# Kernel optimization log

Measured on AMD Instinct MI355X. Metric: run time of the kernel, lower is better.

The kernel has to match this reference:

```python
import jax, jax.numpy as jnp
import numpy as np

TAU = 0.5
EPS = 1e-8


def _mlp(x, W1, b1, W2, b2):
    # torch nn.Linear: y = x @ W.T + b
    h = jax.nn.elu(x @ W1.T + b1)
    return h @ W2.T + b2


def setup_inputs() -> dict:
    key = jax.random.key(0)
    ks = jax.random.split(key, 10)
    N, D = 8192, 256
    gain = 1.414
    std = gain * np.sqrt(2.0 / (D + D))  # xavier_normal_
    inp = {
        "z1": jax.random.normal(ks[0], (N, D), dtype=jnp.float32),
        "z2": jax.random.normal(ks[1], (N, D), dtype=jnp.float32),
        "W1c": std * jax.random.normal(ks[2], (D, D), dtype=jnp.float32),
        "b1c": jnp.zeros((D,), dtype=jnp.float32),
        "W2c": std * jax.random.normal(ks[3], (D, D), dtype=jnp.float32),
        "b2c": jnp.zeros((D,), dtype=jnp.float32),
        "W1k": std * jax.random.normal(ks[4], (D, D), dtype=jnp.float32),
        "b1k": jnp.zeros((D,), dtype=jnp.float32),
        "W2k": std * jax.random.normal(ks[5], (D, D), dtype=jnp.float32),
        "b2k": jnp.zeros((D,), dtype=jnp.float32),
        "cl_size": N,
    }
    return inp


def reference(z1, z2, W1c, b1c, W2c, b2c, W1k, b1k, W2k, b2k, cl_size):
    z1p = _mlp(z1, W1c, b1c, W2c, b2c)  # [N, D]
    z2p = _mlp(z2, W1k, b1k, W2k, b2k)  # [N, D]
    n1 = jnp.linalg.norm(z1p, axis=-1, keepdims=True)  # [N, 1]
    n2 = jnp.linalg.norm(z2p, axis=-1, keepdims=True)  # [N, 1]
    dot = z1p @ z2p.T                                  # [N, N]
    sim = jnp.exp(dot / (n1 * n2.T) / TAU)
    sim = sim / (jnp.sum(sim, axis=1, keepdims=True) + EPS)
    pos = jnp.diagonal(sim)                            # diag(sim * I).sum(-1)
    return -jnp.mean(jnp.log(pos))
```

## Files before the change

kernel.cpp:

```cpp
#include <hip/hip_runtime.h>

typedef __bf16 bf16;
typedef __bf16 bf16x8 __attribute__((ext_vector_type(8)));
typedef __bf16 bf16x4v __attribute__((ext_vector_type(4)));
typedef float  f32x4  __attribute__((ext_vector_type(4)));

#define NROWS 8192
#define DDIM  256
#define TAU_INV 2.0f
#define KAPPA 2.8853900817779268f
#define LN2 0.6931471805599453f
#define EPS 1e-8f

#define AS1C(p) ((const __attribute__((address_space(1))) void*)(p))
#define AS3(p)  ((__attribute__((address_space(3))) void*)(p))

static __device__ __forceinline__ bf16x8 cvt8(f32x4 a, f32x4 b) {
  bf16x8 o;
  o[0] = (bf16)a[0]; o[1] = (bf16)a[1]; o[2] = (bf16)a[2]; o[3] = (bf16)a[3];
  o[4] = (bf16)b[0]; o[5] = (bf16)b[1]; o[6] = (bf16)b[2]; o[7] = (bf16)b[3];
  return o;
}

__global__ __launch_bounds__(256) void cast4_kernel(
    const float* __restrict__ s0, const float* __restrict__ s1,
    const float* __restrict__ s2, const float* __restrict__ s3,
    bf16* __restrict__ dst) {
  const float* s = blockIdx.y == 0 ? s0 : blockIdx.y == 1 ? s1 : blockIdx.y == 2 ? s2 : s3;
  bf16* d = dst + (size_t)blockIdx.y * 65536;
  int i = blockIdx.x * 256 + threadIdx.x;
  f32x4 v = ((const f32x4*)s)[i];
  bf16x4v o;
  o[0] = (bf16)v[0]; o[1] = (bf16)v[1]; o[2] = (bf16)v[2]; o[3] = (bf16)v[3];
  ((bf16x4v*)d)[i] = o;
}

__global__ __launch_bounds__(512, 1) void mlp_norm_kernel(
    const float* __restrict__ z1f, const float* __restrict__ z2f,
    const bf16* __restrict__ wq,
    const float* __restrict__ b1c, const float* __restrict__ b2c,
    const float* __restrict__ b1k, const float* __restrict__ b2k,
    bf16* __restrict__ outA, bf16* __restrict__ outB)
{
  const int view = blockIdx.y;
  const float* xf = view ? z2f : z1f;
  const bf16*  w1 = wq + (size_t)view * 131072;
  const bf16*  w2 = w1 + 65536;
  const float* b1 = view ? b1k : b1c;
  const float* b2 = view ? b2k : b2c;
  bf16* out = view ? outB : outA;
  const float osc = view ? 1.0f : KAPPA;

  __shared__ __align__(16) char xs[64 * 512];
  __shared__ __align__(16) char hs[64 * 512];
  __shared__ float sspart[8][64];

  const int tid  = threadIdx.x;
  const int lane = tid & 63;
  const int w    = tid >> 6;
  const int c    = lane & 15;
  const int g    = lane >> 4;
  const int r0   = blockIdx.x * 64;
  const int colw = w * 32;

#pragma unroll
  for (int k = 0; k < 4; ++k) {
    int gid = k * 512 + tid;
    int row = gid >> 5, cg = gid & 31;
    const f32x4* p = (const f32x4*)(xf + (size_t)(r0 + row) * DDIM + cg * 8);
    *(bf16x8*)(xs + row * 512 + ((cg * 16) ^ ((row & 7) << 4))) = cvt8(p[0], p[1]);
  }
  __syncthreads();

  float b1v[2], b2v[2];
#pragma unroll
  for (int ct = 0; ct < 2; ++ct) {
    b1v[ct] = b1[colw + ct * 16 + c];
    b2v[ct] = b2[colw + ct * 16 + c];
  }

  const int aswz = (c & 7) << 4;
  const bf16* w1base = w1 + (size_t)(colw + c) * DDIM + g * 8;
  const bf16* w2base = w2 + (size_t)(colw + c) * DDIM + g * 8;

  f32x4 acc[2][4];
  const f32x4 fz = {0.f, 0.f, 0.f, 0.f};
#pragma unroll
  for (int ct = 0; ct < 2; ++ct)
#pragma unroll
    for (int mt = 0; mt < 4; ++mt) acc[ct][mt] = fz;

  bf16x8 wcur[2], wnxt[2];
#pragma unroll
  for (int ct = 0; ct < 2; ++ct)
    wcur[ct] = *(const bf16x8*)(w1base + (size_t)ct * 16 * DDIM);
#pragma unroll
  for (int ks = 0; ks < 8; ++ks) {
    if (ks < 7) {
#pragma unroll
      for (int ct = 0; ct < 2; ++ct)
        wnxt[ct] = *(const bf16x8*)(w1base + (size_t)ct * 16 * DDIM + (ks + 1) * 32);
    }
    bf16x8 af[4];
#pragma unroll
    for (int mt = 0; mt < 4; ++mt)
      af[mt] = *(const bf16x8*)(xs + (mt * 16 + c) * 512 + ((ks * 64 + g * 16) ^ aswz));
#pragma unroll
    for (int ct = 0; ct < 2; ++ct)
#pragma unroll
      for (int mt = 0; mt < 4; ++mt)
        acc[ct][mt] = __builtin_amdgcn_mfma_f32_16x16x32_bf16(af[mt], wcur[ct], acc[ct][mt], 0, 0, 0);
#pragma unroll
    for (int ct = 0; ct < 2; ++ct) wcur[ct] = wnxt[ct];
  }

#pragma unroll
  for (int ct = 0; ct < 2; ++ct)
#pragma unroll
    for (int mt = 0; mt < 4; ++mt)
#pragma unroll
      for (int r = 0; r < 4; ++r) {
        float pre = acc[ct][mt][r] + b1v[ct];
        float h = pre > 0.0f ? pre : (__expf(pre) - 1.0f);
        int row = mt * 16 + g * 4 + r;
        int cb = (colw + ct * 16 + c) * 2;
        *(bf16*)(hs + row * 512 + (cb ^ ((row & 7) << 4))) = (bf16)h;
      }
  __syncthreads();

#pragma unroll
  for (int ct = 0; ct < 2; ++ct)
#pragma unroll
    for (int mt = 0; mt < 4; ++mt) acc[ct][mt] = fz;

#pragma unroll
  for (int ct = 0; ct < 2; ++ct)
    wcur[ct] = *(const bf16x8*)(w2base + (size_t)ct * 16 * DDIM);
#pragma unroll
  for (int ks = 0; ks < 8; ++ks) {
    if (ks < 7) {
#pragma unroll
      for (int ct = 0; ct < 2; ++ct)
        wnxt[ct] = *(const bf16x8*)(w2base + (size_t)ct * 16 * DDIM + (ks + 1) * 32);
    }
    bf16x8 af[4];
#pragma unroll
    for (int mt = 0; mt < 4; ++mt)
      af[mt] = *(const bf16x8*)(hs + (mt * 16 + c) * 512 + ((ks * 64 + g * 16) ^ aswz));
#pragma unroll
    for (int ct = 0; ct < 2; ++ct)
#pragma unroll
      for (int mt = 0; mt < 4; ++mt)
        acc[ct][mt] = __builtin_amdgcn_mfma_f32_16x16x32_bf16(af[mt], wcur[ct], acc[ct][mt], 0, 0, 0);
#pragma unroll
    for (int ct = 0; ct < 2; ++ct) wcur[ct] = wnxt[ct];
  }

  float ss[4][4];
#pragma unroll
  for (int mt = 0; mt < 4; ++mt)
#pragma unroll
    for (int r = 0; r < 4; ++r) ss[mt][r] = 0.f;
#pragma unroll
  for (int ct = 0; ct < 2; ++ct)
#pragma unroll
    for (int mt = 0; mt < 4; ++mt)
#pragma unroll
      for (int r = 0; r < 4; ++r) {
        float z = acc[ct][mt][r] + b2v[ct];
        acc[ct][mt][r] = z;
        ss[mt][r] += z * z;
      }
#pragma unroll
  for (int m = 1; m < 16; m <<= 1)
#pragma unroll
    for (int mt = 0; mt < 4; ++mt)
#pragma unroll
      for (int r = 0; r < 4; ++r) ss[mt][r] += __shfl_xor(ss[mt][r], m, 64);

  if (c == 0) {
#pragma unroll
    for (int mt = 0; mt < 4; ++mt)
#pragma unroll
      for (int r = 0; r < 4; ++r) sspart[w][mt * 16 + g * 4 + r] = ss[mt][r];
  }
  __syncthreads();

#pragma unroll
  for (int mt = 0; mt < 4; ++mt)
#pragma unroll
    for (int r = 0; r < 4; ++r) {
      int row = mt * 16 + g * 4 + r;
      float s = (sspart[0][row] + sspart[1][row]) + (sspart[2][row] + sspart[3][row])
              + (sspart[4][row] + sspart[5][row]) + (sspart[6][row] + sspart[7][row]);
      float rinv = osc / sqrtf(s);
#pragma unroll
      for (int ct = 0; ct < 2; ++ct)
        out[(size_t)(r0 + row) * DDIM + colw + ct * 16 + c] = (bf16)(acc[ct][mt][r] * rinv);
    }
}

__global__ __launch_bounds__(256, 2) void lse_kernel(
    const bf16* __restrict__ A, const bf16* __restrict__ B,
    float* __restrict__ partial, float* __restrict__ diagdot)
{
  __shared__ __align__(16) char As[128 * 128];
  __shared__ __align__(16) char Bs[128 * 128];

  const int tid  = threadIdx.x;
  const int lane = tid & 63;
  const int w    = tid >> 6;
  const int c    = lane & 15;
  const int g    = lane >> 4;
  const int brow = blockIdx.y * 128;
  const int bcol = blockIdx.x * 128;
  const int wrow = (w >> 1) * 64;
  const int wcol = (w & 1) * 64;

  f32x4 acc[4][4];
  const f32x4 fz = {0.f, 0.f, 0.f, 0.f};
#pragma unroll
  for (int i = 0; i < 4; ++i)
#pragma unroll
    for (int j = 0; j < 4; ++j) acc[i][j] = fz;

  for (int kt = 0; kt < 4; ++kt) {
#pragma unroll
    for (int it = 0; it < 4; ++it) {
      int slot = it * 256 + tid;
      int row = slot >> 3, q = slot & 7;
      int col = kt * 64 + ((q ^ (row & 7)) * 8);
      __builtin_amdgcn_global_load_lds(AS1C(A + (size_t)(brow + row) * DDIM + col),
                                       AS3(As + (it * 256 + w * 64) * 16), 16, 0, 0);
      __builtin_amdgcn_global_load_lds(AS1C(B + (size_t)(bcol + row) * DDIM + col),
                                       AS3(Bs + (it * 256 + w * 64) * 16), 16, 0, 0);
    }
    __syncthreads();
#pragma unroll
    for (int sk = 0; sk < 2; ++sk) {
      bf16x8 af[4], bfv[4];
#pragma unroll
      for (int mt = 0; mt < 4; ++mt) {
        int rl = wrow + mt * 16 + c;
        af[mt] = *(const bf16x8*)(As + rl * 128 + ((sk * 64 + g * 16) ^ ((rl & 7) << 4)));
      }
#pragma unroll
      for (int ct = 0; ct < 4; ++ct) {
        int rl = wcol + ct * 16 + c;
        bfv[ct] = *(const bf16x8*)(Bs + rl * 128 + ((sk * 64 + g * 16) ^ ((rl & 7) << 4)));
      }
#pragma unroll
      for (int mt = 0; mt < 4; ++mt)
#pragma unroll
        for (int ct = 0; ct < 4; ++ct)
          acc[mt][ct] = __builtin_amdgcn_mfma_f32_16x16x32_bf16(af[mt], bfv[ct], acc[mt][ct], 0, 0, 0);
    }
    __syncthreads();
  }

  if (blockIdx.x == blockIdx.y && (w == 0 || w == 3) && (c >> 2) == g) {
#pragma unroll
    for (int mt = 0; mt < 4; ++mt) {
      f32x4 a = acc[mt][mt];
      int r = c & 3;
      float dv = (r == 0) ? a[0] : (r == 1) ? a[1] : (r == 2) ? a[2] : a[3];
      diagdot[brow + wrow + mt * 16 + c] = dv;
    }
  }

  float rs[4][4];
#pragma unroll
  for (int mt = 0; mt < 4; ++mt)
#pragma unroll
    for (int r = 0; r < 4; ++r) rs[mt][r] = 0.f;
#pragma unroll
  for (int mt = 0; mt < 4; ++mt)
#pragma unroll
    for (int ct = 0; ct < 4; ++ct)
#pragma unroll
      for (int r = 0; r < 4; ++r) rs[mt][r] += __builtin_amdgcn_exp2f(acc[mt][ct][r]);
#pragma unroll
  for (int m = 1; m < 16; m <<= 1)
#pragma unroll
    for (int mt = 0; mt < 4; ++mt)
#pragma unroll
      for (int r = 0; r < 4; ++r) rs[mt][r] += __shfl_xor(rs[mt][r], m, 64);

  if (c == 0) {
    int cb2 = blockIdx.x * 2 + (w & 1);
#pragma unroll
    for (int mt = 0; mt < 4; ++mt)
#pragma unroll
      for (int r = 0; r < 4; ++r) {
        int grow = brow + wrow + mt * 16 + g * 4 + r;
        partial[(size_t)grow * 128 + cb2] = rs[mt][r];
      }
  }
}

__global__ __launch_bounds__(256) void rowfinal_kernel(
    const float* __restrict__ partial, const float* __restrict__ diagdot,
    float* __restrict__ blocksum)
{
  int gid = blockIdx.x * 256 + threadIdx.x;
  int row = gid >> 2, q = gid & 3;
  const f32x4* p = (const f32x4*)(partial + (size_t)row * 128 + q * 32);
  float s = 0.f;
#pragma unroll
  for (int i = 0; i < 8; ++i) {
    f32x4 v = p[i];
    s += (v[0] + v[1]) + (v[2] + v[3]);
  }
  s += __shfl_xor(s, 1, 64);
  s += __shfl_xor(s, 2, 64);
  float term = (q == 0) ? (logf(s + EPS) - diagdot[row] * LN2) : 0.f;
#pragma unroll
  for (int m = 1; m < 64; m <<= 1) term += __shfl_xor(term, m, 64);
  __shared__ float part[4];
  if ((threadIdx.x & 63) == 0) part[threadIdx.x >> 6] = term;
  __syncthreads();
  if (threadIdx.x == 0) blocksum[blockIdx.x] = part[0] + part[1] + part[2] + part[3];
}

__global__ __launch_bounds__(128) void final_kernel(const float* __restrict__ blocksum,
                                                    float* __restrict__ out)
{
  int tid = threadIdx.x;
  float s = blocksum[tid];
#pragma unroll
  for (int m = 1; m < 64; m <<= 1) s += __shfl_xor(s, m, 64);
  __shared__ float p[2];
  if ((tid & 63) == 0) p[tid >> 6] = s;
  __syncthreads();
  if (tid == 0) out[0] = (p[0] + p[1]) * (1.0f / NROWS);
}

extern "C" void kernel_launch(void* const* d_in, const int* in_sizes, int n_in,
                              void* d_out, int out_size, void* d_ws, size_t ws_size,
                              hipStream_t stream) {
  const float* z1  = (const float*)d_in[0];
  const float* z2  = (const float*)d_in[1];
  const float* W1c = (const float*)d_in[2];
  const float* b1c = (const float*)d_in[3];
  const float* W2c = (const float*)d_in[4];
  const float* b2c = (const float*)d_in[5];
  const float* W1k = (const float*)d_in[6];
  const float* b1k = (const float*)d_in[7];
  const float* W2k = (const float*)d_in[8];
  const float* b2k = (const float*)d_in[9];

  char* ws = (char*)d_ws;
  bf16*  aU       = (bf16*)(ws);
  bf16*  bU       = (bf16*)(ws + (size_t)4  * 1024 * 1024);
  float* partial  = (float*)(ws + (size_t)8  * 1024 * 1024);
  float* diagdot  = (float*)(ws + (size_t)12 * 1024 * 1024);
  float* blocksum = (float*)(ws + (size_t)12 * 1024 * 1024 + 64 * 1024);
  bf16*  wq       = (bf16*)(ws + (size_t)13 * 1024 * 1024);

  cast4_kernel<<<dim3(64, 4), 256, 0, stream>>>(W1c, W2c, W1k, W2k, wq);

  mlp_norm_kernel<<<dim3(NROWS / 64, 2), 512, 0, stream>>>(
      z1, z2, wq, b1c, b2c, b1k, b2k, aU, bU);

  lse_kernel<<<dim3(NROWS / 128, NROWS / 128), 256, 0, stream>>>(aU, bU, partial, diagdot);

  rowfinal_kernel<<<128, 256, 0, stream>>>(partial, diagdot, blocksum);
  final_kernel<<<1, 128, 0, stream>>>(blocksum, (float*)d_out);
}
```

Baseline: 75.94 us.

## Quantize normalized embeddings to FP8 and use FP8 MFMA for similarity GEMM

```diff
diff --git a/kernel.cpp b/kernel.cpp
--- a/kernel.cpp
+++ b/kernel.cpp
@@ -1,4 +1,5 @@
 #include <hip/hip_runtime.h>
+#include <hip/hip_fp8.h>
 
 typedef __bf16 bf16;
 typedef __bf16 bf16x8 __attribute__((ext_vector_type(8)));
@@ -20,6 +21,11 @@
   o[0] = (bf16)a[0]; o[1] = (bf16)a[1]; o[2] = (bf16)a[2]; o[3] = (bf16)a[3];
   o[4] = (bf16)b[0]; o[5] = (bf16)b[1]; o[6] = (bf16)b[2]; o[7] = (bf16)b[3];
   return o;
+}
+
+static __device__ __forceinline__ unsigned char f2fp8(float x) {
+  __hip_fp8_e4m3 q(x);
+  return (unsigned char)q.__x;
 }
 
 __global__ __launch_bounds__(256) void cast4_kernel(
@@ -40,7 +46,7 @@
     const bf16* __restrict__ wq,
     const float* __restrict__ b1c, const float* __restrict__ b2c,
     const float* __restrict__ b1k, const float* __restrict__ b2k,
-    bf16* __restrict__ outA, bf16* __restrict__ outB)
+    unsigned char* __restrict__ outA, unsigned char* __restrict__ outB)
 {
   const int view = blockIdx.y;
   const float* xf = view ? z2f : z1f;
@@ -48,7 +54,7 @@
   const bf16*  w2 = w1 + 65536;
   const float* b1 = view ? b1k : b1c;
   const float* b2 = view ? b2k : b2c;
-  bf16* out = view ? outB : outA;
+  unsigned char* out = view ? outB : outA;
   const float osc = view ? 1.0f : KAPPA;
 
   __shared__ __align__(16) char xs[64 * 512];
@@ -196,16 +202,16 @@
       float rinv = osc / sqrtf(s);
 #pragma unroll
       for (int ct = 0; ct < 2; ++ct)
-        out[(size_t)(r0 + row) * DDIM + colw + ct * 16 + c] = (bf16)(acc[ct][mt][r] * rinv);
+        out[(size_t)(r0 + row) * DDIM + colw + ct * 16 + c] = f2fp8(acc[ct][mt][r] * rinv);
     }
 }
 
 __global__ __launch_bounds__(256, 2) void lse_kernel(
-    const bf16* __restrict__ A, const bf16* __restrict__ B,
+    const unsigned char* __restrict__ A, const unsigned char* __restrict__ B,
     float* __restrict__ partial, float* __restrict__ diagdot)
 {
-  __shared__ __align__(16) char As[128 * 128];
-  __shared__ __align__(16) char Bs[128 * 128];
+  __shared__ __align__(16) char As[128 * 64];
+  __shared__ __align__(16) char Bs[128 * 64];
 
   const int tid  = threadIdx.x;
   const int lane = tid & 63;
@@ -226,34 +232,36 @@
 
   for (int kt = 0; kt < 4; ++kt) {
 #pragma unroll
-    for (int it = 0; it < 4; ++it) {
+    for (int it = 0; it < 2; ++it) {
       int slot = it * 256 + tid;
-      int row = slot >> 3, q = slot & 7;
-      int col = kt * 64 + ((q ^ (row & 7)) * 8);
+      int row = slot >> 2, q = slot & 3;
+      int col = kt * 64 + ((q ^ (row & 3)) << 4);
       __builtin_amdgcn_global_load_lds(AS1C(A + (size_t)(brow + row) * DDIM + col),
-                                       AS3(As + (it * 256 + w * 64) * 16), 16, 0, 0);
+                                       AS3(As + slot * 16), 16, 0, 0);
       __builtin_amdgcn_global_load_lds(AS1C(B + (size_t)(bcol + row) * DDIM + col),
-                                       AS3(Bs + (it * 256 + w * 64) * 16), 16, 0, 0);
+                                       AS3(Bs + slot * 16), 16, 0, 0);
     }
     __syncthreads();
 #pragma unroll
     for (int sk = 0; sk < 2; ++sk) {
-      bf16x8 af[4], bfv[4];
+      long af[4], bfv[4];
 #pragma unroll
       for (int mt = 0; mt < 4; ++mt) {
         int rl = wrow + mt * 16 + c;
-        af[mt] = *(const bf16x8*)(As + rl * 128 + ((sk * 64 + g * 16) ^ ((rl & 7) << 4)));
+        af[mt] = *(const long*)(As + rl * 64
+                  + ((((sk << 1) | (g >> 1)) ^ (rl & 3)) << 4) + ((g & 1) << 3));
       }
 #pragma unroll
       for (int ct = 0; ct < 4; ++ct) {
         int rl = wcol + ct * 16 + c;
-        bfv[ct] = *(const bf16x8*)(Bs + rl * 128 + ((sk * 64 + g * 16) ^ ((rl & 7) << 4)));
+        bfv[ct] = *(const long*)(Bs + rl * 64
+                  + ((((sk << 1) | (g >> 1)) ^ (rl & 3)) << 4) + ((g & 1) << 3));
       }
 #pragma unroll
       for (int mt = 0; mt < 4; ++mt)
 #pragma unroll
         for (int ct = 0; ct < 4; ++ct)
-          acc[mt][ct] = __builtin_amdgcn_mfma_f32_16x16x32_bf16(af[mt], bfv[ct], acc[mt][ct], 0, 0, 0);
+          acc[mt][ct] = __builtin_amdgcn_mfma_f32_16x16x32_fp8_fp8(af[mt], bfv[ct], acc[mt][ct], 0, 0, 0);
     }
     __syncthreads();
   }
@@ -350,12 +358,12 @@
   const float* b2k = (const float*)d_in[9];
 
   char* ws = (char*)d_ws;
-  bf16*  aU       = (bf16*)(ws);
-  bf16*  bU       = (bf16*)(ws + (size_t)4  * 1024 * 1024);
-  float* partial  = (float*)(ws + (size_t)8  * 1024 * 1024);
-  float* diagdot  = (float*)(ws + (size_t)12 * 1024 * 1024);
-  float* blocksum = (float*)(ws + (size_t)12 * 1024 * 1024 + 64 * 1024);
-  bf16*  wq       = (bf16*)(ws + (size_t)13 * 1024 * 1024);
+  unsigned char* aU = (unsigned char*)(ws);
+  unsigned char* bU = (unsigned char*)(ws + (size_t)2 * 1024 * 1024);
+  float* partial  = (float*)(ws + (size_t)4  * 1024 * 1024);
+  float* diagdot  = (float*)(ws + (size_t)8  * 1024 * 1024);
+  float* blocksum = (float*)(ws + (size_t)8  * 1024 * 1024 + 64 * 1024);
+  bf16*  wq       = (bf16*)(ws + (size_t)9  * 1024 * 1024);
 
   cast4_kernel<<<dim3(64, 4), 256, 0, stream>>>(W1c, W2c, W1k, W2k, wq);
 
```

New measurement: 80.48 us. 1.06x slower.
